# Performance work log

Measured on AMD Instinct MI355X. Metric: run time of the kernel, lower is better.

## Reference

```python
import jax, jax.numpy as jnp
import numpy as np

DIM = 1024
HEAD_NUM = 8
D_HEAD = DIM // HEAD_NUM
B, S = 4, 2048


def setup_inputs() -> dict:
    key = jax.random.key(0)
    ks = jax.random.split(key, 7)
    scale = 0.02
    return {
        "Q": jax.random.normal(ks[0], (B, S, DIM), dtype=jnp.float32),
        "K": jax.random.normal(ks[1], (B, S, DIM), dtype=jnp.float32),
        "V": jax.random.normal(ks[2], (B, S, DIM), dtype=jnp.float32),
        "W_Q": jax.random.normal(ks[3], (DIM, DIM), dtype=jnp.float32) * scale,
        "W_K": jax.random.normal(ks[4], (DIM, DIM), dtype=jnp.float32) * scale,
        "W_V": jax.random.normal(ks[5], (DIM, DIM), dtype=jnp.float32) * scale,
        "W_O": jax.random.normal(ks[6], (DIM, DIM), dtype=jnp.float32) * scale,
    }


def reference(Q, K, V, W_Q, W_K, W_V, W_O):
    # torch nn.Linear(bias=False): y = x @ W.T
    b, s, d = Q.shape
    h, dh = HEAD_NUM, d // HEAD_NUM

    def proj_split(x, W):
        # split_head: tensor_split along feature dim into h contiguous chunks,
        # stack at dim 1 -> [b, h, s, dh]; equivalent to reshape+transpose.
        y = jnp.einsum('bsd,ed->bse', x, W)
        return y.reshape(b, s, h, dh).transpose(0, 2, 1, 3)

    q = proj_split(Q, W_Q)  # [b,h,s,dh]
    k = proj_split(K, W_K)
    v = proj_split(V, W_V)

    scores = jnp.einsum('bhqd,bhkd->bhqk', q, k) / jnp.sqrt(jnp.float32(dh))
    # FAITHFUL to original: nn.Softmax(dim=1) normalizes over the HEAD axis.
    attn = jax.nn.softmax(scores, axis=1)
    # dropout is identity in eval mode
    ctx = jnp.einsum('bhqk,bhkd->bhqd', attn, v)  # [b,h,s,dh]
    # concat_head: heads concatenated back along feature dim in order
    ctx = ctx.transpose(0, 2, 1, 3).reshape(b, s, d)
    return jnp.einsum('bsd,ed->bse', ctx, W_O)
```

## Files before the change

kernel.cpp:

```cpp
#include <hip/hip_runtime.h>
#include <math.h>
#include <stdint.h>


typedef __attribute__((ext_vector_type(8))) __bf16 bf16x8;
typedef __attribute__((ext_vector_type(4))) __bf16 bf16x4;
typedef __attribute__((ext_vector_type(4))) float  f32x4;
typedef __attribute__((ext_vector_type(2))) unsigned int u32x2;

__device__ __forceinline__ f32x4 mfma16(bf16x8 a, bf16x8 b, f32x4 c) {
    return __builtin_amdgcn_mfma_f32_16x16x32_bf16(a, b, c, 0, 0, 0);
}

__device__ __forceinline__ void cp16(void* lds, const void* g) {
    __builtin_amdgcn_global_load_lds(
        (__attribute__((address_space(1))) void*)(void*)(const_cast<void*>(g)),
        (__attribute__((address_space(3))) void*)lds,
        16, 0, 0);
}

__device__ __forceinline__ float fexp(float x) {
    float r;
    asm("v_exp_f32 %0, %1" : "=v"(r) : "v"(x * 1.44269504088896341f));
    return r;
}
__device__ __forceinline__ float frcp(float x) {
    float r;
    asm("v_rcp_f32 %0, %1" : "=v"(r) : "v"(x));
    return r;
}

__device__ __forceinline__ uint32_t pk2(float a, float b) {
    __bf16 x = (__bf16)a, y = (__bf16)b;
    unsigned short xa = __builtin_bit_cast(unsigned short, x);
    unsigned short yb = __builtin_bit_cast(unsigned short, y);
    return (uint32_t)xa | ((uint32_t)yb << 16);
}
__device__ __forceinline__ float bflo(uint32_t d) {
    return __builtin_bit_cast(float, d << 16);
}
__device__ __forceinline__ float bfhi(uint32_t d) {
    return __builtin_bit_cast(float, d & 0xffff0000u);
}

__global__ void cast4_f32_to_bf16(const float* __restrict__ s0, __bf16* __restrict__ d0,
                                  const float* __restrict__ s1, __bf16* __restrict__ d1,
                                  const float* __restrict__ s2, __bf16* __restrict__ d2,
                                  const float* __restrict__ s3, __bf16* __restrict__ d3,
                                  int n4) {
    const float* s = (blockIdx.y == 0) ? s0 : (blockIdx.y == 1) ? s1
                    : (blockIdx.y == 2) ? s2 : s3;
    __bf16* d = (blockIdx.y == 0) ? d0 : (blockIdx.y == 1) ? d1
               : (blockIdx.y == 2) ? d2 : d3;
    int i = blockIdx.x * blockDim.x + threadIdx.x;
    const int stride = gridDim.x * blockDim.x;
    for (; i < n4; i += stride) {
        float4 f = ((const float4*)s)[i];
        bf16x4 o;
        o[0] = (__bf16)f.x; o[1] = (__bf16)f.y; o[2] = (__bf16)f.z; o[3] = (__bf16)f.w;
        ((bf16x4*)d)[i] = o;
    }
}

__global__ void cast3_f32_to_bf16(const float* __restrict__ s0, __bf16* __restrict__ d0,
                                  const float* __restrict__ s1, __bf16* __restrict__ d1,
                                  const float* __restrict__ s2, __bf16* __restrict__ d2,
                                  int n4) {
    const float* s = (blockIdx.y == 0) ? s0 : (blockIdx.y == 1) ? s1 : s2;
    __bf16* d = (blockIdx.y == 0) ? d0 : (blockIdx.y == 1) ? d1 : d2;
    int i = blockIdx.x * blockDim.x + threadIdx.x;
    const int stride = gridDim.x * blockDim.x;
    for (; i < n4; i += stride) {
        float4 f = ((const float4*)s)[i];
        bf16x4 o;
        o[0] = (__bf16)f.x; o[1] = (__bf16)f.y; o[2] = (__bf16)f.z; o[3] = (__bf16)f.w;
        ((bf16x4*)d)[i] = o;
    }
}

template<int MODE>
__global__ __launch_bounds__(256, 2) void gemm_bt(const __bf16* __restrict__ A,
                                                  const __bf16* __restrict__ Bt,
                                                  void* __restrict__ out,
                                                  float scale)
{
    __shared__ __bf16 As[128 * 32];
    __shared__ __bf16 Bs[128 * 32];
    const int tid  = threadIdx.x;
    const int lane = tid & 63;
    const int u = lane >> 4, v = lane & 15;
    const int w = tid >> 6;
    const int wm = (w >> 1) * 64, wn = (w & 1) * 64;
    const int bid = blockIdx.y * 8 + blockIdx.x;
    const long tM = (long)(bid & 63) * 128;
    const int  tN = (bid >> 6) * 128;

    f32x4 acc[4][4];
#pragma unroll
    for (int i = 0; i < 4; ++i)
#pragma unroll
        for (int j = 0; j < 4; ++j) acc[i][j] = (f32x4){0.f, 0.f, 0.f, 0.f};

    const int c0 = tid, c1 = tid + 256;
    const int ar0 = c0 >> 2, ak0 = (c0 & 3) * 8;
    const int ar1 = c1 >> 2, ak1 = (c1 & 3) * 8;

    const __bf16* Ab = A  + tM * 1024;
    const __bf16* Bb = Bt + (long)tN * 1024;

    for (int k0 = 0; k0 < 1024; k0 += 32) {
        __syncthreads();
        cp16(&As[ar0 * 32 + ak0], Ab + (long)ar0 * 1024 + k0 + ak0);
        cp16(&As[ar1 * 32 + ak1], Ab + (long)ar1 * 1024 + k0 + ak1);
        cp16(&Bs[ar0 * 32 + ak0], Bb + (long)ar0 * 1024 + k0 + ak0);
        cp16(&Bs[ar1 * 32 + ak1], Bb + (long)ar1 * 1024 + k0 + ak1);
        __syncthreads();

        bf16x8 af[4], bfr[4];
#pragma unroll
        for (int i = 0; i < 4; ++i)
            af[i] = *(const bf16x8*)&As[(wm + i * 16 + v) * 32 + u * 8];
#pragma unroll
        for (int j = 0; j < 4; ++j)
            bfr[j] = *(const bf16x8*)&Bs[(wn + j * 16 + v) * 32 + u * 8];
#pragma unroll
        for (int i = 0; i < 4; ++i)
#pragma unroll
            for (int j = 0; j < 4; ++j)
                acc[i][j] = mfma16(af[i], bfr[j], acc[i][j]);
    }

#pragma unroll
    for (int i = 0; i < 4; ++i) {
#pragma unroll
        for (int j = 0; j < 4; ++j) {
            const long row0 = tM + wm + i * 16 + u * 4;
            const int  col  = tN + wn + j * 16 + v;
            if (MODE == 1) {
                float* o = (float*)out;
#pragma unroll
                for (int r = 0; r < 4; ++r)
                    o[(row0 + r) * 1024 + col] = acc[i][j][r];
            } else {
                __bf16* o = (__bf16*)out;
#pragma unroll
                for (int r = 0; r < 4; ++r)
                    o[(row0 + r) * 1024 + col] = (__bf16)(acc[i][j][r] * scale);
            }
        }
    }
}

__global__ __launch_bounds__(256, 2) void qkv_proj(
    const __bf16* __restrict__ xq, const __bf16* __restrict__ xk,
    const __bf16* __restrict__ xv,
    const __bf16* __restrict__ wq, const __bf16* __restrict__ wk,
    const __bf16* __restrict__ wv,
    __bf16* __restrict__ qp, __bf16* __restrict__ kp, __bf16* __restrict__ vtb,
    float qscale)
{
    __shared__ __bf16 As[128 * 32];
    __shared__ __bf16 Bs[128 * 32];
    const int z = blockIdx.z;
    const __bf16* A  = (z == 0) ? xq : (z == 1) ? xk : xv;
    const __bf16* Bt = (z == 0) ? wq : (z == 1) ? wk : wv;
    __bf16* out      = (z == 0) ? qp : (z == 1) ? kp : vtb;
    const float scale = (z == 0) ? qscale : 1.0f;

    const int tid  = threadIdx.x;
    const int lane = tid & 63;
    const int u = lane >> 4, v = lane & 15;
    const int w = tid >> 6;
    const int wm = (w >> 1) * 64, wn = (w & 1) * 64;
    const int bid = blockIdx.y * 8 + blockIdx.x;
    const long tM = (long)(bid & 63) * 128;
    const int  tN = (bid >> 6) * 128;

    f32x4 acc[4][4];
#pragma unroll
    for (int i = 0; i < 4; ++i)
#pragma unroll
        for (int j = 0; j < 4; ++j) acc[i][j] = (f32x4){0.f, 0.f, 0.f, 0.f};

    const int c0 = tid, c1 = tid + 256;
    const int ar0 = c0 >> 2, ak0 = (c0 & 3) * 8;
    const int ar1 = c1 >> 2, ak1 = (c1 & 3) * 8;

    const __bf16* Ab = A  + tM * 1024;
    const __bf16* Bb = Bt + (long)tN * 1024;

    for (int k0 = 0; k0 < 1024; k0 += 32) {
        __syncthreads();
        cp16(&As[ar0 * 32 + ak0], Ab + (long)ar0 * 1024 + k0 + ak0);
        cp16(&As[ar1 * 32 + ak1], Ab + (long)ar1 * 1024 + k0 + ak1);
        cp16(&Bs[ar0 * 32 + ak0], Bb + (long)ar0 * 1024 + k0 + ak0);
        cp16(&Bs[ar1 * 32 + ak1], Bb + (long)ar1 * 1024 + k0 + ak1);
        __syncthreads();

        bf16x8 af[4], bfr[4];
#pragma unroll
        for (int i = 0; i < 4; ++i)
            af[i] = *(const bf16x8*)&As[(wm + i * 16 + v) * 32 + u * 8];
#pragma unroll
        for (int j = 0; j < 4; ++j)
            bfr[j] = *(const bf16x8*)&Bs[(wn + j * 16 + v) * 32 + u * 8];
#pragma unroll
        for (int i = 0; i < 4; ++i)
#pragma unroll
            for (int j = 0; j < 4; ++j)
                acc[i][j] = mfma16(af[i], bfr[j], acc[i][j]);
    }

#pragma unroll
    for (int i = 0; i < 4; ++i) {
#pragma unroll
        for (int j = 0; j < 4; ++j) {
            const long row0 = tM + wm + i * 16 + u * 4;
            const int  col  = tN + wn + j * 16 + v;
            if (z < 2) {
#pragma unroll
                for (int r = 0; r < 4; ++r)
                    out[(row0 + r) * 1024 + col] = (__bf16)(acc[i][j][r] * scale);
            } else {
                const int bidx = (int)(row0 >> 11);
                const int s    = (int)(row0 & 2047);
                const int h = col >> 7, dh = col & 127;
                bf16x4 pkv;
#pragma unroll
                for (int r = 0; r < 4; ++r) pkv[r] = (__bf16)acc[i][j][r];
                *(bf16x4*)&out[((long)(bidx * 8 + h) * 128 + dh) * 2048 + s] = pkv;
            }
        }
    }
}

__global__ __launch_bounds__(512, 2) void fused_attn(
    const __bf16* __restrict__ qp, const __bf16* __restrict__ kp,
    const __bf16* __restrict__ vt, __bf16* __restrict__ ctx)
{
    __shared__ __bf16 Pl[8][32][128];

    const int tid  = threadIdx.x;
    const int w    = tid >> 6;
    const int lane = tid & 63;
    const int u = lane >> 4, v = lane & 15;

    const int g0 = blockIdx.x;
    const int xs = g0 & 7, idx = g0 >> 3;
    const int b  = xs >> 1;
    const int qt = idx * 2 + (xs & 1);
    const int q0 = qt * 32;
    const int h  = w;

    const __bf16* Qb = qp + ((long)b * 2048 + q0) * 1024 + h * 128;
    const __bf16* Kb = kp + (long)b * 2048 * 1024 + h * 128;
    const __bf16* Vb = vt + (long)(b * 8 + h) * 128 * 2048;

    bf16x8 qf[2][4];
#pragma unroll
    for (int qj = 0; qj < 2; ++qj)
#pragma unroll
        for (int kk = 0; kk < 4; ++kk)
            qf[qj][kk] = *(const bf16x8*)&Qb[(long)(qj * 16 + v) * 1024 + kk * 32 + u * 8];

    f32x4 ctxa[8][2];
#pragma unroll
    for (int dt = 0; dt < 8; ++dt)
#pragma unroll
        for (int qj = 0; qj < 2; ++qj) ctxa[dt][qj] = (f32x4){0.f, 0.f, 0.f, 0.f};

    char* PlwBase = (char*)&Pl[w][0][0];
    const char* Pl0 = (const char*)&Pl[0][0][0];
    const int swz = v & 7;

    const int off_g0 = ((w & 1) * 16 + v) * 256
                     + ((((w >> 1) * 2 + (u >> 1)) ^ swz) * 16) + (u & 1) * 8;
    const int off_g1 = ((w & 1) * 16 + v) * 256
                     + (((((w >> 1) + 4) * 2 + (u >> 1)) ^ swz) * 16) + (u & 1) * 8;

    for (int it = 0; it < 16; ++it) {
        const int kt = it * 128;

        bf16x8 kfA[4], kfB[4];
#pragma unroll
        for (int kk = 0; kk < 4; ++kk)
            kfA[kk] = *(const bf16x8*)&Kb[(long)(kt + v) * 1024 + kk * 32 + u * 8];

#pragma unroll
        for (int kp2 = 0; kp2 < 4; ++kp2) {
            const int ki0 = kp2 * 2, ki1 = kp2 * 2 + 1;
#pragma unroll
            for (int kk = 0; kk < 4; ++kk)
                kfB[kk] = *(const bf16x8*)&Kb[(long)(kt + ki1 * 16 + v) * 1024
                                              + kk * 32 + u * 8];
            {
                f32x4 e0 = (f32x4){0.f, 0.f, 0.f, 0.f};
                f32x4 e1 = (f32x4){0.f, 0.f, 0.f, 0.f};
#pragma unroll
                for (int kk = 0; kk < 4; ++kk) {
                    e0 = mfma16(kfA[kk], qf[0][kk], e0);
                    e1 = mfma16(kfA[kk], qf[1][kk], e1);
                }
#pragma unroll
                for (int r = 0; r < 4; ++r) { e0[r] = fexp(e0[r]); e1[r] = fexp(e1[r]); }
                const int choff = (((ki0 * 2 + (u >> 1)) ^ swz) * 16) + (u & 1) * 8;
                u32x2 w0; w0.x = pk2(e0[0], e0[1]); w0.y = pk2(e0[2], e0[3]);
                u32x2 w1; w1.x = pk2(e1[0], e1[1]); w1.y = pk2(e1[2], e1[3]);
                *(u32x2*)(PlwBase + v * 256 + choff) = w0;
                *(u32x2*)(PlwBase + (16 + v) * 256 + choff) = w1;
            }
            if (ki1 < 7) {
#pragma unroll
                for (int kk = 0; kk < 4; ++kk)
                    kfA[kk] = *(const bf16x8*)&Kb[(long)(kt + (ki1 + 1) * 16 + v) * 1024
                                                  + kk * 32 + u * 8];
            }
            {
                f32x4 e0 = (f32x4){0.f, 0.f, 0.f, 0.f};
                f32x4 e1 = (f32x4){0.f, 0.f, 0.f, 0.f};
#pragma unroll
                for (int kk = 0; kk < 4; ++kk) {
                    e0 = mfma16(kfB[kk], qf[0][kk], e0);
                    e1 = mfma16(kfB[kk], qf[1][kk], e1);
                }
#pragma unroll
                for (int r = 0; r < 4; ++r) { e0[r] = fexp(e0[r]); e1[r] = fexp(e1[r]); }
                const int choff = (((ki1 * 2 + (u >> 1)) ^ swz) * 16) + (u & 1) * 8;
                u32x2 w0; w0.x = pk2(e0[0], e0[1]); w0.y = pk2(e0[2], e0[3]);
                u32x2 w1; w1.x = pk2(e1[0], e1[1]); w1.y = pk2(e1[2], e1[3]);
                *(u32x2*)(PlwBase + v * 256 + choff) = w0;
                *(u32x2*)(PlwBase + (16 + v) * 256 + choff) = w1;
            }
        }

        bf16x8 vhoist[8];
#pragma unroll
        for (int dt = 0; dt < 8; ++dt)
            vhoist[dt] = *(const bf16x8*)&Vb[(long)(dt * 16 + v) * 2048 + kt + u * 8];

        __syncthreads();

#pragma unroll
        for (int gp = 0; gp < 2; ++gp) {
            const int off = gp ? off_g1 : off_g0;
            u32x2 dw[8];
#pragma unroll
            for (int wp = 0; wp < 8; ++wp)
                dw[wp] = *(const u32x2*)(Pl0 + wp * 8192 + off);
            f32x4 den = (f32x4){0.f, 0.f, 0.f, 0.f};
#pragma unroll
            for (int wp = 0; wp < 8; ++wp) {
                den[0] += bflo(dw[wp].x); den[1] += bfhi(dw[wp].x);
                den[2] += bflo(dw[wp].y); den[3] += bfhi(dw[wp].y);
            }
            f32x4 rv;
#pragma unroll
            for (int r = 0; r < 4; ++r) rv[r] = frcp(den[r]);
#pragma unroll
            for (int wp = 0; wp < 8; ++wp) {
                u32x2 nw;
                nw.x = pk2(bflo(dw[wp].x) * rv[0], bfhi(dw[wp].x) * rv[1]);
                nw.y = pk2(bflo(dw[wp].y) * rv[2], bfhi(dw[wp].y) * rv[3]);
                *(u32x2*)(const_cast<char*>(Pl0) + wp * 8192 + off) = nw;
            }
        }
        __syncthreads();

        __builtin_amdgcn_s_setprio(1);
#pragma unroll
        for (int kc = 0; kc < 4; ++kc) {
            bf16x8 vg[8];
#pragma unroll
            for (int dt = 0; dt < 8; ++dt)
                vg[dt] = (kc == 0) ? vhoist[dt]
                       : *(const bf16x8*)&Vb[(long)(dt * 16 + v) * 2048
                                             + kt + kc * 32 + u * 8];
            bf16x8 pfr0 = *(const bf16x8*)(PlwBase + v * 256
                                           + (((kc * 4 + u) ^ swz) * 16));
            bf16x8 pfr1 = *(const bf16x8*)(PlwBase + (16 + v) * 256
                                           + (((kc * 4 + u) ^ swz) * 16));
#pragma unroll
            for (int dt = 0; dt < 8; ++dt) {
                ctxa[dt][0] = mfma16(vg[dt], pfr0, ctxa[dt][0]);
                ctxa[dt][1] = mfma16(vg[dt], pfr1, ctxa[dt][1]);
            }
        }
        __builtin_amdgcn_s_setprio(0);
    }

#pragma unroll
    for (int dt = 0; dt < 8; ++dt)
#pragma unroll
        for (int qj = 0; qj < 2; ++qj) {
            bf16x4 o;
#pragma unroll
            for (int r = 0; r < 4; ++r) o[r] = (__bf16)ctxa[dt][qj][r];
            *(bf16x4*)&ctx[((long)b * 2048 + q0 + qj * 16 + v) * 1024
                           + h * 128 + dt * 16 + u * 4] = o;
        }
}

extern "C" void kernel_launch(void* const* d_in, const int* in_sizes, int n_in,
                              void* d_out, int out_size, void* d_ws, size_t ws_size,
                              hipStream_t stream)
{
    const float* Q  = (const float*)d_in[0];
    const float* K  = (const float*)d_in[1];
    const float* V  = (const float*)d_in[2];
    const float* WQ = (const float*)d_in[3];
    const float* WK = (const float*)d_in[4];
    const float* WV = (const float*)d_in[5];
    const float* WO = (const float*)d_in[6];

    __bf16* ws = (__bf16*)d_ws;
    __bf16* wq = ws;
    __bf16* wk = wq + 1048576;
    __bf16* wv = wk + 1048576;
    __bf16* wo = wv + 1048576;
    __bf16* xq = wo + 1048576;
    __bf16* xk = xq + 8388608;
    __bf16* xv = xk + 8388608;
    __bf16* qp = xv + 8388608;
    __bf16* kp = qp + 8388608;
    __bf16* vt = kp + 8388608;
    __bf16* xb = vt + 8388608;

    const float qscale = 0.08838834764831845f;

    cast4_f32_to_bf16<<<dim3(256, 4), 256, 0, stream>>>(
        WQ, wq, WK, wk, WV, wv, WO, wo, 262144);
    cast3_f32_to_bf16<<<dim3(2048, 3), 256, 0, stream>>>(
        Q, xq, K, xk, V, xv, 2097152);
    qkv_proj<<<dim3(8, 64, 3), 256, 0, stream>>>(
        xq, xk, xv, wq, wk, wv, qp, kp, vt, qscale);

    fused_attn<<<256, 512, 0, stream>>>(qp, kp, vt, xb);

    gemm_bt<1><<<dim3(8, 64), 256, 0, stream>>>(xb, wo, (float*)d_out, 1.0f);
}
```

Measured before the change: 488.0 us.

## Double-buffer P tiles to overlap next QK^T/exp with current PV

Splits the attention loop into QK/exp, head-axis normalization and PV stages, and double-buffers the shared P buffer so the QK^T and exp work for the next key tile is issued before the PV MFMAs of the current tile. The goal is to let the compiler and hardware interleave the exp/VALU work with the PV matrix work and hide K/V global load latency across stages. In exchange, LDS use doubles to 128KB per block, which may limit occupancy at two blocks per CU. The early V hoist is also dropped.

```diff
diff --git a/kernel.cpp b/kernel.cpp
--- a/kernel.cpp
+++ b/kernel.cpp
@@ -234,11 +234,122 @@
     }
 }
 
+
+__device__ __forceinline__ void step1_qk(
+    const __bf16* __restrict__ Kb, const bf16x8 (&qf)[2][4],
+    char* PlwBase, int kt, int u, int v, int swz)
+{
+    bf16x8 kfA[4], kfB[4];
+#pragma unroll
+    for (int kk = 0; kk < 4; ++kk)
+        kfA[kk] = *(const bf16x8*)&Kb[(long)(kt + v) * 1024 + kk * 32 + u * 8];
+
+#pragma unroll
+    for (int kp2 = 0; kp2 < 4; ++kp2) {
+        const int ki0 = kp2 * 2, ki1 = kp2 * 2 + 1;
+#pragma unroll
+        for (int kk = 0; kk < 4; ++kk)
+            kfB[kk] = *(const bf16x8*)&Kb[(long)(kt + ki1 * 16 + v) * 1024
+                                          + kk * 32 + u * 8];
+        {
+            f32x4 e0 = (f32x4){0.f, 0.f, 0.f, 0.f};
+            f32x4 e1 = (f32x4){0.f, 0.f, 0.f, 0.f};
+#pragma unroll
+            for (int kk = 0; kk < 4; ++kk) {
+                e0 = mfma16(kfA[kk], qf[0][kk], e0);
+                e1 = mfma16(kfA[kk], qf[1][kk], e1);
+            }
+#pragma unroll
+            for (int r = 0; r < 4; ++r) { e0[r] = fexp(e0[r]); e1[r] = fexp(e1[r]); }
+            const int choff = (((ki0 * 2 + (u >> 1)) ^ swz) * 16) + (u & 1) * 8;
+            u32x2 w0; w0.x = pk2(e0[0], e0[1]); w0.y = pk2(e0[2], e0[3]);
+            u32x2 w1; w1.x = pk2(e1[0], e1[1]); w1.y = pk2(e1[2], e1[3]);
+            *(u32x2*)(PlwBase + v * 256 + choff) = w0;
+            *(u32x2*)(PlwBase + (16 + v) * 256 + choff) = w1;
+        }
+        if (ki1 < 7) {
+#pragma unroll
+            for (int kk = 0; kk < 4; ++kk)
+                kfA[kk] = *(const bf16x8*)&Kb[(long)(kt + (ki1 + 1) * 16 + v) * 1024
+                                              + kk * 32 + u * 8];
+        }
+        {
+            f32x4 e0 = (f32x4){0.f, 0.f, 0.f, 0.f};
+            f32x4 e1 = (f32x4){0.f, 0.f, 0.f, 0.f};
+#pragma unroll
+            for (int kk = 0; kk < 4; ++kk) {
+                e0 = mfma16(kfB[kk], qf[0][kk], e0);
+                e1 = mfma16(kfB[kk], qf[1][kk], e1);
+            }
+#pragma unroll
+            for (int r = 0; r < 4; ++r) { e0[r] = fexp(e0[r]); e1[r] = fexp(e1[r]); }
+            const int choff = (((ki1 * 2 + (u >> 1)) ^ swz) * 16) + (u & 1) * 8;
+            u32x2 w0; w0.x = pk2(e0[0], e0[1]); w0.y = pk2(e0[2], e0[3]);
+            u32x2 w1; w1.x = pk2(e1[0], e1[1]); w1.y = pk2(e1[2], e1[3]);
+            *(u32x2*)(PlwBase + v * 256 + choff) = w0;
+            *(u32x2*)(PlwBase + (16 + v) * 256 + choff) = w1;
+        }
+    }
+}
+
+__device__ __forceinline__ void step2_red(char* Pl0, int off_g0, int off_g1)
+{
+#pragma unroll
+    for (int gp = 0; gp < 2; ++gp) {
+        const int off = gp ? off_g1 : off_g0;
+        u32x2 dw[8];
+#pragma unroll
+        for (int wp = 0; wp < 8; ++wp)
+            dw[wp] = *(const u32x2*)(Pl0 + wp * 8192 + off);
+        f32x4 den = (f32x4){0.f, 0.f, 0.f, 0.f};
+#pragma unroll
+        for (int wp = 0; wp < 8; ++wp) {
+            den[0] += bflo(dw[wp].x); den[1] += bfhi(dw[wp].x);
+            den[2] += bflo(dw[wp].y); den[3] += bfhi(dw[wp].y);
+        }
+        f32x4 rv;
+#pragma unroll
+        for (int r = 0; r < 4; ++r) rv[r] = frcp(den[r]);
+#pragma unroll
+        for (int wp = 0; wp < 8; ++wp) {
+            u32x2 nw;
+            nw.x = pk2(bflo(dw[wp].x) * rv[0], bfhi(dw[wp].x) * rv[1]);
+            nw.y = pk2(bflo(dw[wp].y) * rv[2], bfhi(dw[wp].y) * rv[3]);
+            *(u32x2*)(Pl0 + wp * 8192 + off) = nw;
+        }
+    }
+}
+
+__device__ __forceinline__ void step3_pv(
+    const __bf16* __restrict__ Vb, const char* PlwBase, int kt,
+    f32x4 (&ctxa)[8][2], int u, int v, int swz)
+{
+    __builtin_amdgcn_s_setprio(1);
+#pragma unroll
+    for (int kc = 0; kc < 4; ++kc) {
+        bf16x8 vg[8];
+#pragma unroll
+        for (int dt = 0; dt < 8; ++dt)
+            vg[dt] = *(const bf16x8*)&Vb[(long)(dt * 16 + v) * 2048
+                                         + kt + kc * 32 + u * 8];
+        bf16x8 pfr0 = *(const bf16x8*)(PlwBase + v * 256
+                                       + (((kc * 4 + u) ^ swz) * 16));
+        bf16x8 pfr1 = *(const bf16x8*)(PlwBase + (16 + v) * 256
+                                       + (((kc * 4 + u) ^ swz) * 16));
+#pragma unroll
+        for (int dt = 0; dt < 8; ++dt) {
+            ctxa[dt][0] = mfma16(vg[dt], pfr0, ctxa[dt][0]);
+            ctxa[dt][1] = mfma16(vg[dt], pfr1, ctxa[dt][1]);
+        }
+    }
+    __builtin_amdgcn_s_setprio(0);
+}
+
 __global__ __launch_bounds__(512, 2) void fused_attn(
     const __bf16* __restrict__ qp, const __bf16* __restrict__ kp,
     const __bf16* __restrict__ vt, __bf16* __restrict__ ctx)
 {
-    __shared__ __bf16 Pl[8][32][128];
+    __shared__ __bf16 Pl[2][8][32][128];
 
     const int tid  = threadIdx.x;
     const int w    = tid >> 6;
@@ -269,123 +380,38 @@
 #pragma unroll
         for (int qj = 0; qj < 2; ++qj) ctxa[dt][qj] = (f32x4){0.f, 0.f, 0.f, 0.f};
 
-    char* PlwBase = (char*)&Pl[w][0][0];
-    const char* Pl0 = (const char*)&Pl[0][0][0];
-    const int swz = v & 7;
+    char* PlA  = (char*)&Pl[0][w][0][0];
+    char* PlB  = (char*)&Pl[1][w][0][0];
+    char* Pl0A = (char*)&Pl[0][0][0][0];
+    char* Pl0B = (char*)&Pl[1][0][0][0];
+    const int swz = v & 15 & 7;
 
     const int off_g0 = ((w & 1) * 16 + v) * 256
                      + ((((w >> 1) * 2 + (u >> 1)) ^ swz) * 16) + (u & 1) * 8;
     const int off_g1 = ((w & 1) * 16 + v) * 256
                      + (((((w >> 1) + 4) * 2 + (u >> 1)) ^ swz) * 16) + (u & 1) * 8;
 
-    for (int it = 0; it < 16; ++it) {
-        const int kt = it * 128;
-
-        bf16x8 kfA[4], kfB[4];
-#pragma unroll
-        for (int kk = 0; kk < 4; ++kk)
-            kfA[kk] = *(const bf16x8*)&Kb[(long)(kt + v) * 1024 + kk * 32 + u * 8];
-
-#pragma unroll
-        for (int kp2 = 0; kp2 < 4; ++kp2) {
-            const int ki0 = kp2 * 2, ki1 = kp2 * 2 + 1;
-#pragma unroll
-            for (int kk = 0; kk < 4; ++kk)
-                kfB[kk] = *(const bf16x8*)&Kb[(long)(kt + ki1 * 16 + v) * 1024
-                                              + kk * 32 + u * 8];
-            {
-                f32x4 e0 = (f32x4){0.f, 0.f, 0.f, 0.f};
-                f32x4 e1 = (f32x4){0.f, 0.f, 0.f, 0.f};
-#pragma unroll
-                for (int kk = 0; kk < 4; ++kk) {
-                    e0 = mfma16(kfA[kk], qf[0][kk], e0);
-                    e1 = mfma16(kfA[kk], qf[1][kk], e1);
-                }
-#pragma unroll
-                for (int r = 0; r < 4; ++r) { e0[r] = fexp(e0[r]); e1[r] = fexp(e1[r]); }
-                const int choff = (((ki0 * 2 + (u >> 1)) ^ swz) * 16) + (u & 1) * 8;
-                u32x2 w0; w0.x = pk2(e0[0], e0[1]); w0.y = pk2(e0[2], e0[3]);
-                u32x2 w1; w1.x = pk2(e1[0], e1[1]); w1.y = pk2(e1[2], e1[3]);
-                *(u32x2*)(PlwBase + v * 256 + choff) = w0;
-                *(u32x2*)(PlwBase + (16 + v) * 256 + choff) = w1;
-            }
-            if (ki1 < 7) {
-#pragma unroll
-                for (int kk = 0; kk < 4; ++kk)
-                    kfA[kk] = *(const bf16x8*)&Kb[(long)(kt + (ki1 + 1) * 16 + v) * 1024
-                                                  + kk * 32 + u * 8];
-            }
-            {
-                f32x4 e0 = (f32x4){0.f, 0.f, 0.f, 0.f};
-                f32x4 e1 = (f32x4){0.f, 0.f, 0.f, 0.f};
-#pragma unroll
-                for (int kk = 0; kk < 4; ++kk) {
-                    e0 = mfma16(kfB[kk], qf[0][kk], e0);
-                    e1 = mfma16(kfB[kk], qf[1][kk], e1);
-                }
-#pragma unroll
-                for (int r = 0; r < 4; ++r) { e0[r] = fexp(e0[r]); e1[r] = fexp(e1[r]); }
-                const int choff = (((ki1 * 2 + (u >> 1)) ^ swz) * 16) + (u & 1) * 8;
-                u32x2 w0; w0.x = pk2(e0[0], e0[1]); w0.y = pk2(e0[2], e0[3]);
-                u32x2 w1; w1.x = pk2(e1[0], e1[1]); w1.y = pk2(e1[2], e1[3]);
-                *(u32x2*)(PlwBase + v * 256 + choff) = w0;
-                *(u32x2*)(PlwBase + (16 + v) * 256 + choff) = w1;
-            }
-        }
-
-        bf16x8 vhoist[8];
-#pragma unroll
-        for (int dt = 0; dt < 8; ++dt)
-            vhoist[dt] = *(const bf16x8*)&Vb[(long)(dt * 16 + v) * 2048 + kt + u * 8];
-
-        __syncthreads();
-
-#pragma unroll
-        for (int gp = 0; gp < 2; ++gp) {
-            const int off = gp ? off_g1 : off_g0;
-            u32x2 dw[8];
-#pragma unroll
-            for (int wp = 0; wp < 8; ++wp)
-                dw[wp] = *(const u32x2*)(Pl0 + wp * 8192 + off);
-            f32x4 den = (f32x4){0.f, 0.f, 0.f, 0.f};
-#pragma unroll
-            for (int wp = 0; wp < 8; ++wp) {
-                den[0] += bflo(dw[wp].x); den[1] += bfhi(dw[wp].x);
-                den[2] += bflo(dw[wp].y); den[3] += bfhi(dw[wp].y);
-            }
-            f32x4 rv;
-#pragma unroll
-            for (int r = 0; r < 4; ++r) rv[r] = frcp(den[r]);
-#pragma unroll
-            for (int wp = 0; wp < 8; ++wp) {
-                u32x2 nw;
-                nw.x = pk2(bflo(dw[wp].x) * rv[0], bfhi(dw[wp].x) * rv[1]);
-                nw.y = pk2(bflo(dw[wp].y) * rv[2], bfhi(dw[wp].y) * rv[3]);
-                *(u32x2*)(const_cast<char*>(Pl0) + wp * 8192 + off) = nw;
-            }
-        }
-        __syncthreads();
-
-        __builtin_amdgcn_s_setprio(1);
-#pragma unroll
-        for (int kc = 0; kc < 4; ++kc) {
-            bf16x8 vg[8];
-#pragma unroll
-            for (int dt = 0; dt < 8; ++dt)
-                vg[dt] = (kc == 0) ? vhoist[dt]
-                       : *(const bf16x8*)&Vb[(long)(dt * 16 + v) * 2048
-                                             + kt + kc * 32 + u * 8];
-            bf16x8 pfr0 = *(const bf16x8*)(PlwBase + v * 256
-                                           + (((kc * 4 + u) ^ swz) * 16));
-            bf16x8 pfr1 = *(const bf16x8*)(PlwBase + (16 + v) * 256
-                                           + (((kc * 4 + u) ^ swz) * 16));
-#pragma unroll
-            for (int dt = 0; dt < 8; ++dt) {
-                ctxa[dt][0] = mfma16(vg[dt], pfr0, ctxa[dt][0]);
-                ctxa[dt][1] = mfma16(vg[dt], pfr1, ctxa[dt][1]);
-            }
-        }
-        __builtin_amdgcn_s_setprio(0);
+    step1_qk(Kb, qf, PlA, 0, u, v, swz);
+    __syncthreads();
+    step2_red(Pl0A, off_g0, off_g1);
+    __syncthreads();
+
+#pragma unroll 1
+    for (int it = 0; it < 16; it += 2) {
+        if (it + 1 < 16) step1_qk(Kb, qf, PlB, (it + 1) * 128, u, v, swz);
+        step3_pv(Vb, PlA, it * 128, ctxa, u, v, swz);
+        if (it + 1 < 16) {
+            __syncthreads();
+            step2_red(Pl0B, off_g0, off_g1);
+            __syncthreads();
+        }
+        if (it + 2 < 16) step1_qk(Kb, qf, PlA, (it + 2) * 128, u, v, swz);
+        if (it + 1 < 16) step3_pv(Vb, PlB, (it + 1) * 128, ctxa, u, v, swz);
+        if (it + 2 < 16) {
+            __syncthreads();
+            step2_red(Pl0A, off_g0, off_g1);
+            __syncthreads();
+        }
     }
 
 #pragma unroll
```

Result: slower. 502.3 us (+2.9%).
